# Performance work log

Measured on AMD Instinct MI355X. Metric: run time of the kernel, lower is better.

## Reference

```python
import jax, jax.numpy as jnp
import numpy as np

N_NODES = 100000


def gcn_conv(x, edge_index, W, b):
    """PyG GCNConv: add self-loops, symmetric deg^{-1/2} A deg^{-1/2} aggregation.

    x: [N, Fin], edge_index: [2, E] int (row 0 = src, row 1 = dst).
    Transform first (Fin -> Fout), then gather-normalize-scatter at Fout.
    """
    n = x.shape[0]
    loops = jnp.arange(n, dtype=edge_index.dtype)
    src = jnp.concatenate([edge_index[0], loops])
    dst = jnp.concatenate([edge_index[1], loops])
    # in-degree with self-loops (all edge weights = 1)
    deg = jax.ops.segment_sum(jnp.ones_like(dst, dtype=x.dtype), dst, num_segments=n)
    dinv = jax.lax.rsqrt(deg)  # deg >= 1 thanks to self-loops
    norm = dinv[src] * dinv[dst]  # [E+N]
    h = x @ W  # [N, Fout] dense transform before sparse aggregation
    msgs = norm[:, None] * h[src]  # gather + normalize
    out = jax.ops.segment_sum(msgs, dst, num_segments=n)  # scatter-add
    return out + b


def setup_inputs() -> dict:
    key = jax.random.key(0)
    ks = jax.random.split(key, 8)
    N, E, Fin, H, C = N_NODES, 1600000, 256, 64, 11
    x = jax.random.normal(ks[0], (N, Fin), dtype=jnp.float32)
    edge_index = jax.random.randint(ks[1], (2, E), 0, N, dtype=jnp.int64)
    s1 = 1.0 / np.sqrt(Fin)
    s2 = 1.0 / np.sqrt(H)
    W1 = jax.random.uniform(ks[2], (Fin, H), jnp.float32, -s1, s1)
    b1 = jnp.zeros((H,), jnp.float32)
    W2 = jax.random.uniform(ks[3], (H, H), jnp.float32, -s2, s2)
    b2 = jnp.zeros((H,), jnp.float32)
    Wfc = jax.random.uniform(ks[4], (H, C), jnp.float32, -s2, s2)
    bfc = jax.random.uniform(ks[5], (C,), jnp.float32, -s2, s2)
    return {"x": x, "edge_index": edge_index, "W1": W1, "b1": b1,
            "W2": W2, "b2": b2, "Wfc": Wfc, "bfc": bfc}


def reference(x, edge_index, W1, b1, W2, b2, Wfc, bfc):
    h = jax.nn.relu(gcn_conv(x, edge_index, W1, b1))
    h = jax.nn.relu(gcn_conv(h, edge_index, W2, b2))
    return h @ Wfc + bfc  # [N, 11]
```

## Files before the change

kernel.cpp:

```cpp
#include <hip/hip_runtime.h>
#include <hip/hip_fp16.h>

#define NFEAT 64
#define CE 8192
#define EBUF 4608

typedef _Float16 half8 __attribute__((ext_vector_type(8)));
typedef float f32x4 __attribute__((ext_vector_type(4)));

__device__ __forceinline__ void gll16(const float* g, float* l) {
    __builtin_amdgcn_global_load_lds(
        (const __attribute__((address_space(1))) unsigned int*)g,
        (__attribute__((address_space(3))) unsigned int*)l, 16, 0, 0);
}

__device__ __forceinline__ __half2 bch(unsigned int u) {
    return __builtin_bit_cast(__half2, u);
}

__global__ __launch_bounds__(256) void k_prep(
    const float* __restrict__ W1, __half* __restrict__ Wt1,
    const float* __restrict__ W2, __half* __restrict__ Wt2,
    const int* __restrict__ eiDst, int* __restrict__ hist, int E, int nbkt)
{
    __shared__ int hb[512];
    int bid = blockIdx.x, tid = threadIdx.x;
    if (bid < 64) {
        int idx = bid * 256 + tid;
        int n = idx >> 8, k = idx & 255;
        Wt1[idx] = __float2half(W1[(size_t)k * NFEAT + n]);
    } else if (bid < 80) {
        int idx = (bid - 64) * 256 + tid;
        int n = idx >> 6, k = idx & 63;
        Wt2[idx] = __float2half(W2[(size_t)k * NFEAT + n]);
    } else {
        int c = bid - 80;
        int base = c * CE;
        if (base >= E) return;
        for (int i = tid; i < nbkt; i += 256) hb[i] = 0;
        __syncthreads();
        int hi = min(base + CE, E);
        for (int e = base + tid; e < hi; e += 256)
            atomicAdd(&hb[eiDst[e] >> 8], 1);
        __syncthreads();
        for (int i = tid; i < nbkt; i += 256)
            hist[(size_t)c * nbkt + i] = hb[i];
    }
}

template<int K, bool SCALE>
__global__ __launch_bounds__(256) void k_gemm_x(
    const float* __restrict__ A, const __half* __restrict__ Wt,
    const float* __restrict__ dinv, __half* __restrict__ H, int M)
{
    const int BM = 64, BK = 32;
    __shared__ float As[2 * BM * BK];

    int tid = threadIdx.x;
    int gemmIdx = blockIdx.x;
    if (gemmIdx * BM >= M) return;

    int w = tid >> 6, lane = tid & 63;
    int q = lane >> 4, n16 = lane & 15;
    int m0 = gemmIdx * BM;

    auto stage = [&](int k0, int buf) {
#pragma unroll
        for (int rep = 0; rep < 2; ++rep) {
            int cb = (w * 2 + rep) * 64;
            int s = cb + lane;
            int m = s >> 3;
            int kk = (s & 7) ^ (m & 7);
            int row = m0 + m; if (row > M - 1) row = M - 1;
            gll16(A + (size_t)row * K + k0 + kk * 4,
                  &As[buf * (BM * BK) + cb * 4]);
        }
    };

    stage(0, 0);

    f32x4 acc[4];
#pragma unroll
    for (int nt = 0; nt < 4; ++nt) acc[nt] = (f32x4)(0.f);

    const __half* wp = Wt + (size_t)n16 * K + q * 8;

    const int T = K / BK;
    for (int kt = 0; kt < T; ++kt) {
        __syncthreads();
        if (kt + 1 < T) stage((kt + 1) * BK, (kt + 1) & 1);
        const float* As_ = &As[(kt & 1) * (BM * BK)];

        int ml = w * 16 + n16;
        int e0 = (2 * q) ^ (ml & 7);
        int e1 = (2 * q + 1) ^ (ml & 7);
        float4 f0 = *(const float4*)&As_[(ml * 8 + e0) * 4];
        float4 f1 = *(const float4*)&As_[(ml * 8 + e1) * 4];
        float fv[8] = {f0.x, f0.y, f0.z, f0.w, f1.x, f1.y, f1.z, f1.w};
        half8 ahi, alo;
#pragma unroll
        for (int j = 0; j < 8; ++j) {
            _Float16 hi = (_Float16)fv[j];
            ahi[j] = hi;
            alo[j] = (_Float16)(fv[j] - (float)hi);
        }
#pragma unroll
        for (int nt = 0; nt < 4; ++nt) {
            uint4 u = *(const uint4*)(wp + (size_t)(nt * 16) * K + kt * BK);
            half8 b = __builtin_bit_cast(half8, u);
            acc[nt] = __builtin_amdgcn_mfma_f32_16x16x32_f16(ahi, b, acc[nt], 0, 0, 0);
            acc[nt] = __builtin_amdgcn_mfma_f32_16x16x32_f16(alo, b, acc[nt], 0, 0, 0);
        }
        __syncthreads();
    }

#pragma unroll
    for (int reg = 0; reg < 4; ++reg) {
        int row = m0 + w * 16 + q * 4 + reg;
        if (row < M) {
            float di = SCALE ? dinv[row] : 1.0f;
#pragma unroll
            for (int nt = 0; nt < 4; ++nt)
                H[(size_t)row * NFEAT + nt * 16 + n16] =
                    __float2half(di * acc[nt][reg]);
        }
    }
}

__global__ __launch_bounds__(256) void k_scanB(int* __restrict__ hist,
                                               int* __restrict__ cntB,
                                               int nchk, int nbkt) {
    __shared__ int hb[256];
    int b = blockIdx.x, tid = threadIdx.x;
    int v = (tid < nchk) ? hist[(size_t)tid * nbkt + b] : 0;
    hb[tid] = v;
    __syncthreads();
    for (int off = 1; off < 256; off <<= 1) {
        int t = (tid >= off) ? hb[tid - off] : 0;
        __syncthreads();
        if (tid >= off) hb[tid] += t;
        __syncthreads();
    }
    if (tid < nchk) hist[(size_t)tid * nbkt + b] = hb[tid] - v;
    if (tid == 255) cntB[b] = hb[255];
}

__global__ __launch_bounds__(256) void k_scanC(const int* __restrict__ cntB,
                                               int* __restrict__ bb, int nbkt) {
    __shared__ int hb[256];
    int tid = threadIdx.x;
    int i0 = 2 * tid, i1 = 2 * tid + 1;
    int a0 = (i0 < nbkt) ? cntB[i0] : 0;
    int a1 = (i1 < nbkt) ? cntB[i1] : 0;
    hb[tid] = a0 + a1;
    __syncthreads();
    for (int off = 1; off < 256; off <<= 1) {
        int t = (tid >= off) ? hb[tid - off] : 0;
        __syncthreads();
        if (tid >= off) hb[tid] += t;
        __syncthreads();
    }
    int excl = hb[tid] - (a0 + a1);
    if (i0 <= nbkt) bb[i0] = excl;
    if (i1 <= nbkt) bb[i1] = excl + a0;
}

__global__ __launch_bounds__(256) void k_scatter(
    const int* __restrict__ ei, const int* __restrict__ hist,
    const int* __restrict__ bb, int2* __restrict__ E2, int E, int nbkt)
{
    __shared__ int ptr[512];
    int c = blockIdx.x, tid = threadIdx.x;
    for (int i = tid; i < nbkt; i += 256)
        ptr[i] = bb[i] + hist[(size_t)c * nbkt + i];
    __syncthreads();
    int base = c * CE, hi = min(base + CE, E);
    for (int e = base + tid; e < hi; e += 256) {
        int s = ei[e];
        int d = ei[(size_t)E + e];
        int p = atomicAdd(&ptr[d >> 8], 1);
        E2[p] = make_int2(s, d);
    }
}

__global__ __launch_bounds__(256) void k_csr(
    const int2* __restrict__ E2, const int* __restrict__ bb,
    int* __restrict__ rowptr, float* __restrict__ dinv, int* __restrict__ col,
    int N, int E)
{
    __shared__ int2 ebuf[EBUF];
    __shared__ int cnt[256];
    __shared__ float dl[256];
    int b = blockIdx.x, tid = threadIdx.x;
    int e0 = bb[b], e1 = bb[b + 1], ne = e1 - e0;
    int nL = min(ne, EBUF);

    cnt[tid] = 0;
    __syncthreads();
    for (int i = tid; i < nL; i += 256) {
        int2 e = E2[e0 + i];
        ebuf[i] = e;
        atomicAdd(&cnt[e.y & 255], 1);
    }
    for (int i = nL + tid; i < ne; i += 256) {
        int2 e = E2[e0 + i];
        atomicAdd(&cnt[e.y & 255], 1);
    }
    __syncthreads();
    int c = cnt[tid];
    dl[tid] = rsqrtf((float)(c + 1));
    for (int off = 1; off < 256; off <<= 1) {
        int t = (tid >= off) ? cnt[tid - off] : 0;
        __syncthreads();
        if (tid >= off) cnt[tid] += t;
        __syncthreads();
    }
    int excl = cnt[tid] - c;
    int node = b * 256 + tid;
    if (node < N) {
        rowptr[node] = e0 + excl;
        dinv[node] = dl[tid];
    }
    if (b == 0 && tid == 0) rowptr[N] = E;
    __syncthreads();
    cnt[tid] = excl;
    __syncthreads();
    for (int i = tid; i < nL; i += 256) {
        int2 e = ebuf[i];
        int p = atomicAdd(&cnt[e.y & 255], 1);
        col[e0 + p] = e.x;
    }
    for (int i = nL + tid; i < ne; i += 256) {
        int2 e = E2[e0 + i];
        int p = atomicAdd(&cnt[e.y & 255], 1);
        col[e0 + p] = e.x;
    }
}

__global__ __launch_bounds__(256) void k_ag1g2(
    const __half* __restrict__ h, const int* __restrict__ rowptr,
    const int* __restrict__ col, const float* __restrict__ dinv,
    const float* __restrict__ b1, const __half* __restrict__ Wt2,
    __half* __restrict__ H2, int n)
{
    __shared__ float Bs[64][68];
    int tid = threadIdx.x;
    int w = tid >> 6, lane = tid & 63;
    int li = lane & 7, fi = li << 3;
    int slot = (w << 3) | (lane >> 3);

    const __half* hp = h + fi;
    auto ld = [&](int src) { return *(const uint4*)(hp + (size_t)src * NFEAT); };

#pragma unroll
    for (int hf = 0; hf < 2; ++hf) {
        int lr = hf * 32 + slot;
        int r = blockIdx.x * 64 + lr;
        float t0 = 0.f, t1 = 0.f, t2 = 0.f, t3 = 0.f,
              t4 = 0.f, t5 = 0.f, t6 = 0.f, t7 = 0.f;
        if (r < n) {
            float a0 = 0.f, a1 = 0.f, a2 = 0.f, a3 = 0.f,
                  a4 = 0.f, a5 = 0.f, a6 = 0.f, a7 = 0.f;
            auto addu = [&](uint4 u) {
                float2 f0 = __half22float2(bch(u.x));
                float2 f1 = __half22float2(bch(u.y));
                float2 f2 = __half22float2(bch(u.z));
                float2 f3 = __half22float2(bch(u.w));
                a0 += f0.x; a1 += f0.y; a2 += f1.x; a3 += f1.y;
                a4 += f2.x; a5 += f2.y; a6 += f3.x; a7 += f3.y;
            };
            auto p2 = [&](uint4 u0, uint4 u1) {
                uint4 s;
                s.x = __builtin_bit_cast(unsigned int, __hadd2(bch(u0.x), bch(u1.x)));
                s.y = __builtin_bit_cast(unsigned int, __hadd2(bch(u0.y), bch(u1.y)));
                s.z = __builtin_bit_cast(unsigned int, __hadd2(bch(u0.z), bch(u1.z)));
                s.w = __builtin_bit_cast(unsigned int, __hadd2(bch(u0.w), bch(u1.w)));
                addu(s);
            };
            int beg = rowptr[r], end = rowptr[r + 1];
            addu(ld(r));
            int j = beg;
            for (; j + 3 < end; j += 4) {
                uint4 u0 = ld(col[j]);
                uint4 u1 = ld(col[j + 1]);
                uint4 u2 = ld(col[j + 2]);
                uint4 u3 = ld(col[j + 3]);
                p2(u0, u1);
                p2(u2, u3);
            }
            for (; j < end; ++j) addu(ld(col[j]));
            float di = dinv[r];
            t0 = fmaxf(b1[fi + 0] + di * a0, 0.f);
            t1 = fmaxf(b1[fi + 1] + di * a1, 0.f);
            t2 = fmaxf(b1[fi + 2] + di * a2, 0.f);
            t3 = fmaxf(b1[fi + 3] + di * a3, 0.f);
            t4 = fmaxf(b1[fi + 4] + di * a4, 0.f);
            t5 = fmaxf(b1[fi + 5] + di * a5, 0.f);
            t6 = fmaxf(b1[fi + 6] + di * a6, 0.f);
            t7 = fmaxf(b1[fi + 7] + di * a7, 0.f);
        }
        *(float4*)&Bs[lr][fi]     = make_float4(t0, t1, t2, t3);
        *(float4*)&Bs[lr][fi + 4] = make_float4(t4, t5, t6, t7);
    }
    __syncthreads();

    int q = lane >> 4, n16 = lane & 15;
    f32x4 acc[4];
#pragma unroll
    for (int nt = 0; nt < 4; ++nt) acc[nt] = (f32x4)(0.f);
    const __half* wp = Wt2 + (size_t)n16 * 64 + q * 8;

#pragma unroll
    for (int kt = 0; kt < 2; ++kt) {
        const float* ap = &Bs[w * 16 + n16][kt * 32 + q * 8];
        float4 f0 = *(const float4*)ap;
        float4 f1 = *(const float4*)(ap + 4);
        float fv[8] = {f0.x, f0.y, f0.z, f0.w, f1.x, f1.y, f1.z, f1.w};
        half8 ahi, alo;
#pragma unroll
        for (int j = 0; j < 8; ++j) {
            _Float16 hi = (_Float16)fv[j];
            ahi[j] = hi;
            alo[j] = (_Float16)(fv[j] - (float)hi);
        }
#pragma unroll
        for (int nt = 0; nt < 4; ++nt) {
            uint4 u = *(const uint4*)(wp + (size_t)(nt * 16) * 64 + kt * 32);
            half8 b = __builtin_bit_cast(half8, u);
            acc[nt] = __builtin_amdgcn_mfma_f32_16x16x32_f16(ahi, b, acc[nt], 0, 0, 0);
            acc[nt] = __builtin_amdgcn_mfma_f32_16x16x32_f16(alo, b, acc[nt], 0, 0, 0);
        }
    }
#pragma unroll
    for (int reg = 0; reg < 4; ++reg) {
        int row = blockIdx.x * 64 + w * 16 + q * 4 + reg;
        if (row < n) {
            float di = dinv[row];
#pragma unroll
            for (int nt = 0; nt < 4; ++nt)
                H2[(size_t)row * NFEAT + nt * 16 + n16] =
                    __float2half(di * acc[nt][reg]);
        }
    }
}

__global__ __launch_bounds__(256) void k_aggr2(
    const __half* __restrict__ h, const int* __restrict__ rowptr,
    const int* __restrict__ col, const float* __restrict__ dinv,
    const float* __restrict__ bias, const float* __restrict__ Wfc,
    const float* __restrict__ bfc, float* __restrict__ out, int n)
{
    __shared__ float Wl[NFEAT * 11 + 11];
    int tid = threadIdx.x;
    for (int i = tid; i < NFEAT * 11; i += 256) Wl[i] = Wfc[i];
    if (tid < 11) Wl[NFEAT * 11 + tid] = bfc[tid];
    __syncthreads();

    int lane = tid & 63;
    int li = lane & 7;
    int fi = li << 3;
    int r = blockIdx.x * 32 + ((tid >> 6) << 3) + (lane >> 3);
    bool valid = r < n;

    int beg = 0, end = 0;
    if (valid) { beg = rowptr[r]; end = rowptr[r + 1]; }

    const __half* hp = h + fi;
    auto ld = [&](int src) { return *(const uint4*)(hp + (size_t)src * NFEAT); };

    float a0 = 0.f, a1 = 0.f, a2 = 0.f, a3 = 0.f,
          a4 = 0.f, a5 = 0.f, a6 = 0.f, a7 = 0.f;
    auto addu = [&](uint4 u) {
        float2 f0 = __half22float2(bch(u.x));
        float2 f1 = __half22float2(bch(u.y));
        float2 f2 = __half22float2(bch(u.z));
        float2 f3 = __half22float2(bch(u.w));
        a0 += f0.x; a1 += f0.y; a2 += f1.x; a3 += f1.y;
        a4 += f2.x; a5 += f2.y; a6 += f3.x; a7 += f3.y;
    };
    auto p2 = [&](uint4 u0, uint4 u1) {
        uint4 s;
        s.x = __builtin_bit_cast(unsigned int, __hadd2(bch(u0.x), bch(u1.x)));
        s.y = __builtin_bit_cast(unsigned int, __hadd2(bch(u0.y), bch(u1.y)));
        s.z = __builtin_bit_cast(unsigned int, __hadd2(bch(u0.z), bch(u1.z)));
        s.w = __builtin_bit_cast(unsigned int, __hadd2(bch(u0.w), bch(u1.w)));
        addu(s);
    };

    if (valid) addu(ld(r));
    int j = beg;
    for (; j + 3 < end; j += 4) {
        uint4 u0 = ld(col[j]);
        uint4 u1 = ld(col[j + 1]);
        uint4 u2 = ld(col[j + 2]);
        uint4 u3 = ld(col[j + 3]);
        p2(u0, u1);
        p2(u2, u3);
    }
    for (; j < end; ++j) addu(ld(col[j]));

    if (!valid) return;
    float di = dinv[r];
    float t0 = fmaxf(bias[fi + 0] + di * a0, 0.f);
    float t1 = fmaxf(bias[fi + 1] + di * a1, 0.f);
    float t2 = fmaxf(bias[fi + 2] + di * a2, 0.f);
    float t3 = fmaxf(bias[fi + 3] + di * a3, 0.f);
    float t4 = fmaxf(bias[fi + 4] + di * a4, 0.f);
    float t5 = fmaxf(bias[fi + 5] + di * a5, 0.f);
    float t6 = fmaxf(bias[fi + 6] + di * a6, 0.f);
    float t7 = fmaxf(bias[fi + 7] + di * a7, 0.f);

#pragma unroll
    for (int c = 0; c < 11; ++c) {
        const float* wc = &Wl[fi * 11 + c];
        float p = t0 * wc[0] + t1 * wc[11] + t2 * wc[22] + t3 * wc[33]
                + t4 * wc[44] + t5 * wc[55] + t6 * wc[66] + t7 * wc[77];
        p += __shfl_xor(p, 1, 64);
        p += __shfl_xor(p, 2, 64);
        p += __shfl_xor(p, 4, 64);
        if (li == 0) out[(size_t)r * 11 + c] = p + Wl[NFEAT * 11 + c];
    }
}

extern "C" void kernel_launch(void* const* d_in, const int* in_sizes, int n_in,
                              void* d_out, int out_size, void* d_ws, size_t ws_size,
                              hipStream_t stream) {
    const float* x   = (const float*)d_in[0];
    const int*   ei  = (const int*)d_in[1];
    const float* W1  = (const float*)d_in[2];
    const float* b1  = (const float*)d_in[3];
    const float* W2  = (const float*)d_in[4];
    const float* b2  = (const float*)d_in[5];
    const float* Wfc = (const float*)d_in[6];
    const float* bfc = (const float*)d_in[7];
    float* out = (float*)d_out;

    const int Fin = 256;
    int N = in_sizes[0] / Fin;
    int E = in_sizes[1] / 2;

    char* ws = (char*)d_ws;
    size_t off = 0;
    auto alloc = [&](size_t bytes) { void* p = ws + off; off = (off + bytes + 255) & ~(size_t)255; return p; };
    int*    rowptr = (int*)   alloc((size_t)(N + 1) * 4);
    float*  dinv   = (float*) alloc((size_t)N * 4);
    int*    col    = (int*)   alloc((size_t)E * 4);
    __half* Wt1    = (__half*)alloc((size_t)64 * 256 * 2);
    __half* Wt2    = (__half*)alloc((size_t)64 * 64 * 2);
    __half* A      = (__half*)alloc((size_t)N * NFEAT * 2);
    __half* H2     = (__half*)alloc((size_t)N * NFEAT * 2);

    int NBKT = (N + 255) >> 8;
    int NCHK = (E + CE - 1) / CE;

    int2* E2   = (int2*)alloc((size_t)E * 8);
    int*  hist = (int*) alloc((size_t)NCHK * NBKT * 4);
    int*  bb   = (int*) alloc((size_t)(NBKT + 1) * 4);
    int*  cntB = (int*) alloc((size_t)NBKT * 4);

    int gb = (N + 63) / 64;
    int gA = (N + 31) / 32;

    k_prep<<<80 + NCHK, 256, 0, stream>>>(W1, Wt1, W2, Wt2, ei + E, hist, E, NBKT);

    k_scanB<<<NBKT, 256, 0, stream>>>(hist, cntB, NCHK, NBKT);
    k_scanC<<<1, 256, 0, stream>>>(cntB, bb, NBKT);
    k_scatter<<<NCHK, 256, 0, stream>>>(ei, hist, bb, E2, E, NBKT);
    k_csr<<<NBKT, 256, 0, stream>>>(E2, bb, rowptr, dinv, col, N, E);

    k_gemm_x<256, true><<<gb, 256, 0, stream>>>(x, Wt1, dinv, A, N);

    k_ag1g2<<<gb, 256, 0, stream>>>(A, rowptr, col, dinv, b1, Wt2, H2, N);

    k_aggr2<<<gA, 256, 0, stream>>>(H2, rowptr, col, dinv, b2, Wfc, bfc, out, N);
}
```

Measured before the change: 327.3 us.

## Stage edge scatter through LDS, fold bucket scan into consumers, simplify GEMM loads

```diff
diff --git a/kernel.cpp b/kernel.cpp
--- a/kernel.cpp
+++ b/kernel.cpp
@@ -7,12 +7,6 @@
 
 typedef _Float16 half8 __attribute__((ext_vector_type(8)));
 typedef float f32x4 __attribute__((ext_vector_type(4)));
-
-__device__ __forceinline__ void gll16(const float* g, float* l) {
-    __builtin_amdgcn_global_load_lds(
-        (const __attribute__((address_space(1))) unsigned int*)g,
-        (__attribute__((address_space(3))) unsigned int*)l, 16, 0, 0);
-}
 
 __device__ __forceinline__ __half2 bch(unsigned int u) {
     return __builtin_bit_cast(__half2, u);
@@ -48,85 +42,6 @@
     }
 }
 
-template<int K, bool SCALE>
-__global__ __launch_bounds__(256) void k_gemm_x(
-    const float* __restrict__ A, const __half* __restrict__ Wt,
-    const float* __restrict__ dinv, __half* __restrict__ H, int M)
-{
-    const int BM = 64, BK = 32;
-    __shared__ float As[2 * BM * BK];
-
-    int tid = threadIdx.x;
-    int gemmIdx = blockIdx.x;
-    if (gemmIdx * BM >= M) return;
-
-    int w = tid >> 6, lane = tid & 63;
-    int q = lane >> 4, n16 = lane & 15;
-    int m0 = gemmIdx * BM;
-
-    auto stage = [&](int k0, int buf) {
-#pragma unroll
-        for (int rep = 0; rep < 2; ++rep) {
-            int cb = (w * 2 + rep) * 64;
-            int s = cb + lane;
-            int m = s >> 3;
-            int kk = (s & 7) ^ (m & 7);
-            int row = m0 + m; if (row > M - 1) row = M - 1;
-            gll16(A + (size_t)row * K + k0 + kk * 4,
-                  &As[buf * (BM * BK) + cb * 4]);
-        }
-    };
-
-    stage(0, 0);
-
-    f32x4 acc[4];
-#pragma unroll
-    for (int nt = 0; nt < 4; ++nt) acc[nt] = (f32x4)(0.f);
-
-    const __half* wp = Wt + (size_t)n16 * K + q * 8;
-
-    const int T = K / BK;
-    for (int kt = 0; kt < T; ++kt) {
-        __syncthreads();
-        if (kt + 1 < T) stage((kt + 1) * BK, (kt + 1) & 1);
-        const float* As_ = &As[(kt & 1) * (BM * BK)];
-
-        int ml = w * 16 + n16;
-        int e0 = (2 * q) ^ (ml & 7);
-        int e1 = (2 * q + 1) ^ (ml & 7);
-        float4 f0 = *(const float4*)&As_[(ml * 8 + e0) * 4];
-        float4 f1 = *(const float4*)&As_[(ml * 8 + e1) * 4];
-        float fv[8] = {f0.x, f0.y, f0.z, f0.w, f1.x, f1.y, f1.z, f1.w};
-        half8 ahi, alo;
-#pragma unroll
-        for (int j = 0; j < 8; ++j) {
-            _Float16 hi = (_Float16)fv[j];
-            ahi[j] = hi;
-            alo[j] = (_Float16)(fv[j] - (float)hi);
-        }
-#pragma unroll
-        for (int nt = 0; nt < 4; ++nt) {
-            uint4 u = *(const uint4*)(wp + (size_t)(nt * 16) * K + kt * BK);
-            half8 b = __builtin_bit_cast(half8, u);
-            acc[nt] = __builtin_amdgcn_mfma_f32_16x16x32_f16(ahi, b, acc[nt], 0, 0, 0);
-            acc[nt] = __builtin_amdgcn_mfma_f32_16x16x32_f16(alo, b, acc[nt], 0, 0, 0);
-        }
-        __syncthreads();
-    }
-
-#pragma unroll
-    for (int reg = 0; reg < 4; ++reg) {
-        int row = m0 + w * 16 + q * 4 + reg;
-        if (row < M) {
-            float di = SCALE ? dinv[row] : 1.0f;
-#pragma unroll
-            for (int nt = 0; nt < 4; ++nt)
-                H[(size_t)row * NFEAT + nt * 16 + n16] =
-                    __float2half(di * acc[nt][reg]);
-        }
-    }
-}
-
 __global__ __launch_bounds__(256) void k_scanB(int* __restrict__ hist,
                                                int* __restrict__ cntB,
                                                int nchk, int nbkt) {
@@ -145,10 +60,82 @@
     if (tid == 255) cntB[b] = hb[255];
 }
 
-__global__ __launch_bounds__(256) void k_scanC(const int* __restrict__ cntB,
-                                               int* __restrict__ bb, int nbkt) {
+__global__ __launch_bounds__(256) void k_scatter(
+    const int* __restrict__ ei, const int* __restrict__ hist,
+    const int* __restrict__ cntB, int2* __restrict__ E2, int E, int nbkt)
+{
+    __shared__ int2 ebuf[CE];
+    __shared__ int lofs[512];
+    __shared__ int gbase[512];
+    __shared__ int cur[512];
     __shared__ int hb[256];
-    int tid = threadIdx.x;
+    int c = blockIdx.x, tid = threadIdx.x;
+    int base = c * CE, hi = min(base + CE, E), ne = hi - base;
+
+    for (int i = tid; i < nbkt; i += 256) cur[i] = 0;
+    __syncthreads();
+    for (int e = base + tid; e < hi; e += 256)
+        atomicAdd(&cur[ei[(size_t)E + e] >> 8], 1);
+    __syncthreads();
+
+    int i0 = 2 * tid, i1 = 2 * tid + 1;
+    int a0 = (i0 < nbkt) ? cur[i0] : 0;
+    int a1 = (i1 < nbkt) ? cur[i1] : 0;
+    hb[tid] = a0 + a1;
+    __syncthreads();
+    for (int off = 1; off < 256; off <<= 1) {
+        int t = (tid >= off) ? hb[tid - off] : 0;
+        __syncthreads();
+        if (tid >= off) hb[tid] += t;
+        __syncthreads();
+    }
+    int excl = hb[tid] - (a0 + a1);
+    if (i0 < nbkt) lofs[i0] = excl;
+    if (i1 < nbkt) lofs[i1] = excl + a0;
+
+    int b0 = (i0 < nbkt) ? cntB[i0] : 0;
+    int b1 = (i1 < nbkt) ? cntB[i1] : 0;
+    hb[tid] = b0 + b1;
+    __syncthreads();
+    for (int off = 1; off < 256; off <<= 1) {
+        int t = (tid >= off) ? hb[tid - off] : 0;
+        __syncthreads();
+        if (tid >= off) hb[tid] += t;
+        __syncthreads();
+    }
+    int excl2 = hb[tid] - (b0 + b1);
+    if (i0 < nbkt) gbase[i0] = excl2 + hist[(size_t)c * nbkt + i0];
+    if (i1 < nbkt) gbase[i1] = excl2 + b0 + hist[(size_t)c * nbkt + i1];
+
+    for (int i = tid; i < nbkt; i += 256) cur[i] = lofs[i];
+    __syncthreads();
+    for (int e = base + tid; e < hi; e += 256) {
+        int s = ei[e];
+        int d = ei[(size_t)E + e];
+        int p = atomicAdd(&cur[d >> 8], 1);
+        ebuf[p] = make_int2(s, d);
+    }
+    __syncthreads();
+
+    for (int i = tid; i < ne; i += 256) {
+        int2 e = ebuf[i];
+        int b = e.y >> 8;
+        E2[gbase[b] + (i - lofs[b])] = e;
+    }
+}
+
+__global__ __launch_bounds__(256) void k_csr(
+    const int2* __restrict__ E2, const int* __restrict__ cntB,
+    int* __restrict__ rowptr, float* __restrict__ dinv, int* __restrict__ col,
+    int N, int E, int nbkt)
+{
+    __shared__ int2 ebuf[EBUF];
+    __shared__ int cnt[256];
+    __shared__ float dl[256];
+    __shared__ int bbL[512];
+    __shared__ int hb[256];
+    int b = blockIdx.x, tid = threadIdx.x;
+
     int i0 = 2 * tid, i1 = 2 * tid + 1;
     int a0 = (i0 < nbkt) ? cntB[i0] : 0;
     int a1 = (i1 < nbkt) ? cntB[i1] : 0;
@@ -161,38 +148,13 @@
         __syncthreads();
     }
     int excl = hb[tid] - (a0 + a1);
-    if (i0 <= nbkt) bb[i0] = excl;
-    if (i1 <= nbkt) bb[i1] = excl + a0;
-}
-
-__global__ __launch_bounds__(256) void k_scatter(
-    const int* __restrict__ ei, const int* __restrict__ hist,
-    const int* __restrict__ bb, int2* __restrict__ E2, int E, int nbkt)
-{
-    __shared__ int ptr[512];
-    int c = blockIdx.x, tid = threadIdx.x;
-    for (int i = tid; i < nbkt; i += 256)
-        ptr[i] = bb[i] + hist[(size_t)c * nbkt + i];
-    __syncthreads();
-    int base = c * CE, hi = min(base + CE, E);
-    for (int e = base + tid; e < hi; e += 256) {
-        int s = ei[e];
-        int d = ei[(size_t)E + e];
-        int p = atomicAdd(&ptr[d >> 8], 1);
-        E2[p] = make_int2(s, d);
-    }
-}
-
-__global__ __launch_bounds__(256) void k_csr(
-    const int2* __restrict__ E2, const int* __restrict__ bb,
-    int* __restrict__ rowptr, float* __restrict__ dinv, int* __restrict__ col,
-    int N, int E)
-{
-    __shared__ int2 ebuf[EBUF];
-    __shared__ int cnt[256];
-    __shared__ float dl[256];
-    int b = blockIdx.x, tid = threadIdx.x;
-    int e0 = bb[b], e1 = bb[b + 1], ne = e1 - e0;
+    if (i0 < nbkt) bbL[i0] = excl;
+    if (i1 < nbkt) bbL[i1] = excl + a0;
+    __syncthreads();
+
+    int e0 = bbL[b];
+    int e1 = (b == nbkt - 1) ? E : bbL[b + 1];
+    int ne = e1 - e0;
     int nL = min(ne, EBUF);
 
     cnt[tid] = 0;
@@ -215,15 +177,15 @@
         if (tid >= off) cnt[tid] += t;
         __syncthreads();
     }
-    int excl = cnt[tid] - c;
+    int texcl = cnt[tid] - c;
     int node = b * 256 + tid;
     if (node < N) {
-        rowptr[node] = e0 + excl;
+        rowptr[node] = e0 + texcl;
         dinv[node] = dl[tid];
     }
     if (b == 0 && tid == 0) rowptr[N] = E;
     __syncthreads();
-    cnt[tid] = excl;
+    cnt[tid] = texcl;
     __syncthreads();
     for (int i = tid; i < nL; i += 256) {
         int2 e = ebuf[i];
@@ -234,6 +196,59 @@
         int2 e = E2[e0 + i];
         int p = atomicAdd(&cnt[e.y & 255], 1);
         col[e0 + p] = e.x;
+    }
+}
+
+__global__ __launch_bounds__(256) void k_gemm1(
+    const float* __restrict__ A, const __half* __restrict__ Wt,
+    const float* __restrict__ dinv, __half* __restrict__ H, int M)
+{
+    const int K = 256;
+    int tid = threadIdx.x;
+    int w = tid >> 6, lane = tid & 63;
+    int q = lane >> 4, n16 = lane & 15;
+    int m0 = blockIdx.x * 64;
+
+    int arow = m0 + w * 16 + n16;
+    if (arow > M - 1) arow = M - 1;
+    const float* ap = A + (size_t)arow * K + q * 8;
+    const __half* wp = Wt + (size_t)n16 * K + q * 8;
+
+    f32x4 acc[4];
+#pragma unroll
+    for (int nt = 0; nt < 4; ++nt) acc[nt] = (f32x4)(0.f);
+
+#pragma unroll
+    for (int kt = 0; kt < 8; ++kt) {
+        float4 f0 = *(const float4*)(ap + kt * 32);
+        float4 f1 = *(const float4*)(ap + kt * 32 + 4);
+        float fv[8] = {f0.x, f0.y, f0.z, f0.w, f1.x, f1.y, f1.z, f1.w};
+        half8 ahi, alo;
+#pragma unroll
+        for (int j = 0; j < 8; ++j) {
+            _Float16 hi = (_Float16)fv[j];
+            ahi[j] = hi;
+            alo[j] = (_Float16)(fv[j] - (float)hi);
+        }
+#pragma unroll
+        for (int nt = 0; nt < 4; ++nt) {
+            uint4 u = *(const uint4*)(wp + (size_t)(nt * 16) * K + kt * 32);
+            half8 b = __builtin_bit_cast(half8, u);
+            acc[nt] = __builtin_amdgcn_mfma_f32_16x16x32_f16(ahi, b, acc[nt], 0, 0, 0);
+            acc[nt] = __builtin_amdgcn_mfma_f32_16x16x32_f16(alo, b, acc[nt], 0, 0, 0);
+        }
+    }
+
+#pragma unroll
+    for (int reg = 0; reg < 4; ++reg) {
+        int row = m0 + w * 16 + q * 4 + reg;
+        if (row < M) {
+            float di = dinv[row];
+#pragma unroll
+            for (int nt = 0; nt < 4; ++nt)
+                H[(size_t)row * NFEAT + nt * 16 + n16] =
+                    __float2half(di * acc[nt][reg]);
+        }
     }
 }
 
@@ -455,7 +470,6 @@
 
     int2* E2   = (int2*)alloc((size_t)E * 8);
     int*  hist = (int*) alloc((size_t)NCHK * NBKT * 4);
-    int*  bb   = (int*) alloc((size_t)(NBKT + 1) * 4);
     int*  cntB = (int*) alloc((size_t)NBKT * 4);
 
     int gb = (N + 63) / 64;
@@ -464,11 +478,10 @@
     k_prep<<<80 + NCHK, 256, 0, stream>>>(W1, Wt1, W2, Wt2, ei + E, hist, E, NBKT);
 
     k_scanB<<<NBKT, 256, 0, stream>>>(hist, cntB, NCHK, NBKT);
-    k_scanC<<<1, 256, 0, stream>>>(cntB, bb, NBKT);
-    k_scatter<<<NCHK, 256, 0, stream>>>(ei, hist, bb, E2, E, NBKT);
-    k_csr<<<NBKT, 256, 0, stream>>>(E2, bb, rowptr, dinv, col, N, E);
-
-    k_gemm_x<256, true><<<gb, 256, 0, stream>>>(x, Wt1, dinv, A, N);
+    k_scatter<<<NCHK, 256, 0, stream>>>(ei, hist, cntB, E2, E, NBKT);
+    k_csr<<<NBKT, 256, 0, stream>>>(E2, cntB, rowptr, dinv, col, N, E, NBKT);
+
+    k_gemm1<<<gb, 256, 0, stream>>>(x, Wt1, dinv, A, N);
 
     k_ag1g2<<<gb, 256, 0, stream>>>(A, rowptr, col, dinv, b1, Wt2, H2, N);
 
```

Result: no change. 331.9 us (+1.4%).
